# Performance work log

Hardware: AMD Instinct MI355X
Metric: run time of the kernel (lower is better)

Reference implementation:

```python
import jax, jax.numpy as jnp
import numpy as np

N = 1_000_000
C = 128
B = 16  # number of instances (batch segments)
EPS = 1e-5


def setup_inputs() -> dict:
    key = jax.random.key(0)
    k1, k2 = jax.random.split(key)
    x = jax.random.normal(k1, (N, C), dtype=jnp.float32)
    batch_idx = jnp.sort(jax.random.randint(k2, (N,), 0, B, dtype=jnp.int32))
    weight = jnp.ones((1, C), dtype=jnp.float32)
    bias = jnp.zeros((1, C), dtype=jnp.float32)
    return {"x": x, "batch_idx": batch_idx, "weight": weight, "bias": bias}


def reference(x, batch_idx, weight, bias):
    # per-instance counts [B, 1]
    cnt = jax.ops.segment_sum(jnp.ones((x.shape[0], 1), x.dtype), batch_idx,
                              num_segments=B)
    cnt = jnp.maximum(cnt, 1.0)
    # segment mean [B, C]
    mean = jax.ops.segment_sum(x, batch_idx, num_segments=B) / cnt
    centered = x - mean[batch_idx]               # broadcast-add of -mean
    # segment mean of squared centered features -> per-instance variance [B, C]
    var = jax.ops.segment_sum(centered * centered, batch_idx, num_segments=B) / cnt
    instd = 1.0 / jnp.sqrt(var + EPS)            # [B, C]
    # broadcast-multiply, then affine
    return centered * instd[batch_idx] * weight + bias
```

## Files before the change

kernel.cpp:

```cpp
#include <hip/hip_runtime.h>

#define CC 128
#define BSEG 16
#define EPSV 1e-5f
#define ROWS_PER_BLOCK 512
#define NORM_GRID 2048

typedef float v4f __attribute__((ext_vector_type(4)));

__device__ __forceinline__ v4f vmax0(v4f a)
{
    v4f r; r.x = fmaxf(a.x, 0.f); r.y = fmaxf(a.y, 0.f);
    r.z = fmaxf(a.z, 0.f); r.w = fmaxf(a.w, 0.f); return r;
}
__device__ __forceinline__ v4f vrsqrt_eps(v4f a)
{
    v4f r; r.x = rsqrtf(a.x + EPSV); r.y = rsqrtf(a.y + EPSV);
    r.z = rsqrtf(a.z + EPSV); r.w = rsqrtf(a.w + EPSV); return r;
}

__global__ __launch_bounds__(256) void ms_stats(const float* __restrict__ x,
                                                const int* __restrict__ bidx,
                                                int n,
                                                float* __restrict__ sum,
                                                float* __restrict__ sumsq,
                                                float* __restrict__ cnt)
{
    const int r0 = blockIdx.x * ROWS_PER_BLOCK;
    if (r0 >= n) return;
    const int rend = min(r0 + ROWS_PER_BLOCK, n);
    const int tq = threadIdx.x & 31;
    const int tr = threadIdx.x >> 5;

    const int seg_first = bidx[r0];
    const int seg_last  = bidx[rend - 1];

    v4f s = {0.f, 0.f, 0.f, 0.f};
    v4f q = {0.f, 0.f, 0.f, 0.f};

    if (seg_first == seg_last) {
        int r = r0 + tr;
        for (; r + 8 < rend; r += 16) {
            const v4f a = *reinterpret_cast<const v4f*>(x + (size_t)r * CC + tq * 4);
            const v4f b = *reinterpret_cast<const v4f*>(x + (size_t)(r + 8) * CC + tq * 4);
            s += a; q += a * a;
            s += b; q += b * b;
        }
        if (r < rend) {
            const v4f a = *reinterpret_cast<const v4f*>(x + (size_t)r * CC + tq * 4);
            s += a; q += a * a;
        }
        __shared__ float red[8][8][32];
        red[tr][0][tq] = s.x; red[tr][1][tq] = s.y; red[tr][2][tq] = s.z; red[tr][3][tq] = s.w;
        red[tr][4][tq] = q.x; red[tr][5][tq] = q.y; red[tr][6][tq] = q.z; red[tr][7][tq] = q.w;
        __syncthreads();
        const int j = threadIdx.x >> 5;
        float acc = 0.f;
        #pragma unroll
        for (int k = 0; k < 8; ++k) acc += red[k][j][tq];
        const int ch = tq * 4 + (j & 3);
        atomicAdd(((j < 4) ? sum : sumsq) + seg_first * CC + ch, acc);
        if (threadIdx.x == 0)
            atomicAdd(cnt + seg_first, (float)(rend - r0));
    } else {
        int cur = -1;
        float rows = 0.f;
        for (int r = r0 + tr; r < rend; r += 8) {
            const int seg = bidx[r];
            if (seg != cur) {
                if (cur >= 0) {
                    float* sd = sum   + cur * CC + tq * 4;
                    float* qd = sumsq + cur * CC + tq * 4;
                    atomicAdd(sd + 0, s.x); atomicAdd(sd + 1, s.y);
                    atomicAdd(sd + 2, s.z); atomicAdd(sd + 3, s.w);
                    atomicAdd(qd + 0, q.x); atomicAdd(qd + 1, q.y);
                    atomicAdd(qd + 2, q.z); atomicAdd(qd + 3, q.w);
                    if (tq == 0) atomicAdd(cnt + cur, rows);
                    s = (v4f){0.f, 0.f, 0.f, 0.f};
                    q = (v4f){0.f, 0.f, 0.f, 0.f};
                    rows = 0.f;
                }
                cur = seg;
            }
            const v4f a = *reinterpret_cast<const v4f*>(x + (size_t)r * CC + tq * 4);
            s += a; q += a * a;
            rows += 1.f;
        }
        if (cur >= 0) {
            float* sd = sum   + cur * CC + tq * 4;
            float* qd = sumsq + cur * CC + tq * 4;
            atomicAdd(sd + 0, s.x); atomicAdd(sd + 1, s.y);
            atomicAdd(sd + 2, s.z); atomicAdd(sd + 3, s.w);
            atomicAdd(qd + 0, q.x); atomicAdd(qd + 1, q.y);
            atomicAdd(qd + 2, q.z); atomicAdd(qd + 3, q.w);
            if (tq == 0) atomicAdd(cnt + cur, rows);
        }
    }
}

__global__ __launch_bounds__(256) void ms_norm(const float* __restrict__ x,
                                               const int* __restrict__ bidx,
                                               const float* __restrict__ sum,
                                               const float* __restrict__ sumsq,
                                               const float* __restrict__ cnt,
                                               const float* __restrict__ w,
                                               const float* __restrict__ bias,
                                               float* __restrict__ out,
                                               int n)
{
    const int npairs = n * 16;
    const int chunk  = (npairs + (int)gridDim.x - 1) / (int)gridDim.x;
    const int hi     = npairs - (int)blockIdx.x * chunk;
    if (hi <= 0) return;
    const int lo     = max(hi - chunk, 0);
    const int tid    = (int)threadIdx.x;

    const int c0 = ((hi + tid) & 15) * 8;
    const v4f w0 = *reinterpret_cast<const v4f*>(w + c0);
    const v4f w1 = *reinterpret_cast<const v4f*>(w + c0 + 4);
    const v4f b0 = *reinterpret_cast<const v4f*>(bias + c0);
    const v4f b1 = *reinterpret_cast<const v4f*>(bias + c0 + 4);

    int cur = -1;
    v4f sc0, sc1, sh0, sh1;

    for (int p = hi - 256 + tid; p >= lo; p -= 256) {
        const int r   = p >> 4;
        const int seg = bidx[r];
        if (seg != cur) {
            cur = seg;
            const int gi  = seg * CC + c0;
            const v4f su0 = *reinterpret_cast<const v4f*>(sum + gi);
            const v4f su1 = *reinterpret_cast<const v4f*>(sum + gi + 4);
            const v4f sq0 = *reinterpret_cast<const v4f*>(sumsq + gi);
            const v4f sq1 = *reinterpret_cast<const v4f*>(sumsq + gi + 4);
            const float rn = 1.0f / fmaxf(cnt[seg], 1.0f);
            const v4f m0 = su0 * rn;
            const v4f m1 = su1 * rn;
            const v4f is0 = vrsqrt_eps(vmax0(sq0 * rn - m0 * m0));
            const v4f is1 = vrsqrt_eps(vmax0(sq1 * rn - m1 * m1));
            sc0 = is0 * w0; sc1 = is1 * w1;
            sh0 = b0 - m0 * sc0; sh1 = b1 - m1 * sc1;
        }
        const float* px = x + (size_t)p * 8;
        const v4f a = *reinterpret_cast<const v4f*>(px);
        const v4f b = *reinterpret_cast<const v4f*>(px + 4);
        v4f o0, o1;
        o0.x = fmaf(a.x, sc0.x, sh0.x); o0.y = fmaf(a.y, sc0.y, sh0.y);
        o0.z = fmaf(a.z, sc0.z, sh0.z); o0.w = fmaf(a.w, sc0.w, sh0.w);
        o1.x = fmaf(b.x, sc1.x, sh1.x); o1.y = fmaf(b.y, sc1.y, sh1.y);
        o1.z = fmaf(b.z, sc1.z, sh1.z); o1.w = fmaf(b.w, sc1.w, sh1.w);
        float* po = out + (size_t)p * 8;
        __builtin_nontemporal_store(o0, reinterpret_cast<v4f*>(po));
        __builtin_nontemporal_store(o1, reinterpret_cast<v4f*>(po + 4));
    }
}

extern "C" void kernel_launch(void* const* d_in, const int* in_sizes, int n_in,
                              void* d_out, int out_size, void* d_ws, size_t ws_size,
                              hipStream_t stream)
{
    const float* x    = (const float*)d_in[0];
    const int*   bidx = (const int*)d_in[1];
    const float* w    = (const float*)d_in[2];
    const float* bias = (const float*)d_in[3];
    float* out = (float*)d_out;
    const int n = in_sizes[1];

    float* ws    = (float*)d_ws;
    float* sum   = ws;
    float* sumsq = ws + BSEG * CC;
    float* cnt   = ws + 2 * BSEG * CC;

    (void)hipMemsetAsync(d_ws, 0, (size_t)(2 * BSEG * CC + BSEG) * sizeof(float), stream);

    const int g1 = (n + ROWS_PER_BLOCK - 1) / ROWS_PER_BLOCK;
    ms_stats<<<g1, 256, 0, stream>>>(x, bidx, n, sum, sumsq, cnt);
    ms_norm<<<NORM_GRID, 256, 0, stream>>>(x, bidx, sum, sumsq, cnt, w, bias, out, n);
}
```

Before: 345.2 us.

## Precompute per-segment scale/shift in LDS and unroll grid-stride normalize loop

Each norm block first computes the scale and shift for all 16 segments and 128 channels into shared memory. It then processes the tensor with a grid-stride loop unrolled four times, walking backward, with loads hoisted ahead of the FMAs. This removes the per-thread branch that recomputed stats whenever a segment changed and exposes more memory-level parallelism. The cost is a 2048-element prologue per block and a less contiguous per-block access pattern than the old chunked layout.

```diff
diff --git a/kernel.cpp b/kernel.cpp
--- a/kernel.cpp
+++ b/kernel.cpp
@@ -7,17 +7,6 @@
 #define NORM_GRID 2048
 
 typedef float v4f __attribute__((ext_vector_type(4)));
-
-__device__ __forceinline__ v4f vmax0(v4f a)
-{
-    v4f r; r.x = fmaxf(a.x, 0.f); r.y = fmaxf(a.y, 0.f);
-    r.z = fmaxf(a.z, 0.f); r.w = fmaxf(a.w, 0.f); return r;
-}
-__device__ __forceinline__ v4f vrsqrt_eps(v4f a)
-{
-    v4f r; r.x = rsqrtf(a.x + EPSV); r.y = rsqrtf(a.y + EPSV);
-    r.z = rsqrtf(a.z + EPSV); r.w = rsqrtf(a.w + EPSV); return r;
-}
 
 __global__ __launch_bounds__(256) void ms_stats(const float* __restrict__ x,
                                                 const int* __restrict__ bidx,
@@ -108,51 +97,104 @@
                                                float* __restrict__ out,
                                                int n)
 {
-    const int npairs = n * 16;
-    const int chunk  = (npairs + (int)gridDim.x - 1) / (int)gridDim.x;
-    const int hi     = npairs - (int)blockIdx.x * chunk;
-    if (hi <= 0) return;
-    const int lo     = max(hi - chunk, 0);
-    const int tid    = (int)threadIdx.x;
-
-    const int c0 = ((hi + tid) & 15) * 8;
-    const v4f w0 = *reinterpret_cast<const v4f*>(w + c0);
-    const v4f w1 = *reinterpret_cast<const v4f*>(w + c0 + 4);
-    const v4f b0 = *reinterpret_cast<const v4f*>(bias + c0);
-    const v4f b1 = *reinterpret_cast<const v4f*>(bias + c0 + 4);
-
-    int cur = -1;
-    v4f sc0, sc1, sh0, sh1;
-
-    for (int p = hi - 256 + tid; p >= lo; p -= 256) {
-        const int r   = p >> 4;
-        const int seg = bidx[r];
-        if (seg != cur) {
-            cur = seg;
-            const int gi  = seg * CC + c0;
-            const v4f su0 = *reinterpret_cast<const v4f*>(sum + gi);
-            const v4f su1 = *reinterpret_cast<const v4f*>(sum + gi + 4);
-            const v4f sq0 = *reinterpret_cast<const v4f*>(sumsq + gi);
-            const v4f sq1 = *reinterpret_cast<const v4f*>(sumsq + gi + 4);
-            const float rn = 1.0f / fmaxf(cnt[seg], 1.0f);
-            const v4f m0 = su0 * rn;
-            const v4f m1 = su1 * rn;
-            const v4f is0 = vrsqrt_eps(vmax0(sq0 * rn - m0 * m0));
-            const v4f is1 = vrsqrt_eps(vmax0(sq1 * rn - m1 * m1));
-            sc0 = is0 * w0; sc1 = is1 * w1;
-            sh0 = b0 - m0 * sc0; sh1 = b1 - m1 * sc1;
-        }
-        const float* px = x + (size_t)p * 8;
-        const v4f a = *reinterpret_cast<const v4f*>(px);
-        const v4f b = *reinterpret_cast<const v4f*>(px + 4);
-        v4f o0, o1;
-        o0.x = fmaf(a.x, sc0.x, sh0.x); o0.y = fmaf(a.y, sc0.y, sh0.y);
-        o0.z = fmaf(a.z, sc0.z, sh0.z); o0.w = fmaf(a.w, sc0.w, sh0.w);
-        o1.x = fmaf(b.x, sc1.x, sh1.x); o1.y = fmaf(b.y, sc1.y, sh1.y);
-        o1.z = fmaf(b.z, sc1.z, sh1.z); o1.w = fmaf(b.w, sc1.w, sh1.w);
-        float* po = out + (size_t)p * 8;
-        __builtin_nontemporal_store(o0, reinterpret_cast<v4f*>(po));
-        __builtin_nontemporal_store(o1, reinterpret_cast<v4f*>(po + 4));
+    __shared__ v4f s_scale[BSEG * 32];
+    __shared__ v4f s_shift[BSEG * 32];
+    for (int i = threadIdx.x; i < BSEG * CC; i += 256) {
+        const int b = i >> 7;
+        const int c = i & (CC - 1);
+        const float nn   = fmaxf(cnt[b], 1.0f);
+        const float mean = sum[i] / nn;
+        const float var  = fmaxf(sumsq[i] / nn - mean * mean, 0.0f);
+        const float sc   = rsqrtf(var + EPSV) * w[c];
+        reinterpret_cast<float*>(s_scale)[i] = sc;
+        reinterpret_cast<float*>(s_shift)[i] = fmaf(-mean, sc, bias[c]);
+    }
+    __syncthreads();
+
+    const int total = n * 16;
+    const int T     = (int)(gridDim.x * blockDim.x);
+
+    int p = total - 1 - (int)(blockIdx.x * blockDim.x + threadIdx.x);
+
+    for (; p >= 3 * T; p -= 4 * T) {
+        const int p0 = p, p1 = p - T, p2 = p - 2 * T, p3 = p - 3 * T;
+        const int g0 = bidx[p0 >> 4];
+        const int g1 = bidx[p1 >> 4];
+        const int g2 = bidx[p2 >> 4];
+        const int g3 = bidx[p3 >> 4];
+        const v4f a0 = reinterpret_cast<const v4f*>(x)[2 * (size_t)p0];
+        const v4f b0 = reinterpret_cast<const v4f*>(x)[2 * (size_t)p0 + 1];
+        const v4f a1 = reinterpret_cast<const v4f*>(x)[2 * (size_t)p1];
+        const v4f b1 = reinterpret_cast<const v4f*>(x)[2 * (size_t)p1 + 1];
+        const v4f a2 = reinterpret_cast<const v4f*>(x)[2 * (size_t)p2];
+        const v4f b2 = reinterpret_cast<const v4f*>(x)[2 * (size_t)p2 + 1];
+        const v4f a3 = reinterpret_cast<const v4f*>(x)[2 * (size_t)p3];
+        const v4f b3 = reinterpret_cast<const v4f*>(x)[2 * (size_t)p3 + 1];
+
+        {
+            const int q2i = (p0 & 15) * 2;
+            const v4f sca = s_scale[g0 * 32 + q2i], scb = s_scale[g0 * 32 + q2i + 1];
+            const v4f sha = s_shift[g0 * 32 + q2i], shb = s_shift[g0 * 32 + q2i + 1];
+            v4f oa, ob;
+            oa.x = fmaf(a0.x, sca.x, sha.x); oa.y = fmaf(a0.y, sca.y, sha.y);
+            oa.z = fmaf(a0.z, sca.z, sha.z); oa.w = fmaf(a0.w, sca.w, sha.w);
+            ob.x = fmaf(b0.x, scb.x, shb.x); ob.y = fmaf(b0.y, scb.y, shb.y);
+            ob.z = fmaf(b0.z, scb.z, shb.z); ob.w = fmaf(b0.w, scb.w, shb.w);
+            __builtin_nontemporal_store(oa, reinterpret_cast<v4f*>(out) + 2 * (size_t)p0);
+            __builtin_nontemporal_store(ob, reinterpret_cast<v4f*>(out) + 2 * (size_t)p0 + 1);
+        }
+        {
+            const int q2i = (p1 & 15) * 2;
+            const v4f sca = s_scale[g1 * 32 + q2i], scb = s_scale[g1 * 32 + q2i + 1];
+            const v4f sha = s_shift[g1 * 32 + q2i], shb = s_shift[g1 * 32 + q2i + 1];
+            v4f oa, ob;
+            oa.x = fmaf(a1.x, sca.x, sha.x); oa.y = fmaf(a1.y, sca.y, sha.y);
+            oa.z = fmaf(a1.z, sca.z, sha.z); oa.w = fmaf(a1.w, sca.w, sha.w);
+            ob.x = fmaf(b1.x, scb.x, shb.x); ob.y = fmaf(b1.y, scb.y, shb.y);
+            ob.z = fmaf(b1.z, scb.z, shb.z); ob.w = fmaf(b1.w, scb.w, shb.w);
+            __builtin_nontemporal_store(oa, reinterpret_cast<v4f*>(out) + 2 * (size_t)p1);
+            __builtin_nontemporal_store(ob, reinterpret_cast<v4f*>(out) + 2 * (size_t)p1 + 1);
+        }
+        {
+            const int q2i = (p2 & 15) * 2;
+            const v4f sca = s_scale[g2 * 32 + q2i], scb = s_scale[g2 * 32 + q2i + 1];
+            const v4f sha = s_shift[g2 * 32 + q2i], shb = s_shift[g2 * 32 + q2i + 1];
+            v4f oa, ob;
+            oa.x = fmaf(a2.x, sca.x, sha.x); oa.y = fmaf(a2.y, sca.y, sha.y);
+            oa.z = fmaf(a2.z, sca.z, sha.z); oa.w = fmaf(a2.w, sca.w, sha.w);
+            ob.x = fmaf(b2.x, scb.x, shb.x); ob.y = fmaf(b2.y, scb.y, shb.y);
+            ob.z = fmaf(b2.z, scb.z, shb.z); ob.w = fmaf(b2.w, scb.w, shb.w);
+            __builtin_nontemporal_store(oa, reinterpret_cast<v4f*>(out) + 2 * (size_t)p2);
+            __builtin_nontemporal_store(ob, reinterpret_cast<v4f*>(out) + 2 * (size_t)p2 + 1);
+        }
+        {
+            const int q2i = (p3 & 15) * 2;
+            const v4f sca = s_scale[g3 * 32 + q2i], scb = s_scale[g3 * 32 + q2i + 1];
+            const v4f sha = s_shift[g3 * 32 + q2i], shb = s_shift[g3 * 32 + q2i + 1];
+            v4f oa, ob;
+            oa.x = fmaf(a3.x, sca.x, sha.x); oa.y = fmaf(a3.y, sca.y, sha.y);
+            oa.z = fmaf(a3.z, sca.z, sha.z); oa.w = fmaf(a3.w, sca.w, sha.w);
+            ob.x = fmaf(b3.x, scb.x, shb.x); ob.y = fmaf(b3.y, scb.y, shb.y);
+            ob.z = fmaf(b3.z, scb.z, shb.z); ob.w = fmaf(b3.w, scb.w, shb.w);
+            __builtin_nontemporal_store(oa, reinterpret_cast<v4f*>(out) + 2 * (size_t)p3);
+            __builtin_nontemporal_store(ob, reinterpret_cast<v4f*>(out) + 2 * (size_t)p3 + 1);
+        }
+    }
+
+    for (; p >= 0; p -= T) {
+        const int g = bidx[p >> 4];
+        const v4f a = reinterpret_cast<const v4f*>(x)[2 * (size_t)p];
+        const v4f b = reinterpret_cast<const v4f*>(x)[2 * (size_t)p + 1];
+        const int q2i = (p & 15) * 2;
+        const v4f sca = s_scale[g * 32 + q2i], scb = s_scale[g * 32 + q2i + 1];
+        const v4f sha = s_shift[g * 32 + q2i], shb = s_shift[g * 32 + q2i + 1];
+        v4f oa, ob;
+        oa.x = fmaf(a.x, sca.x, sha.x); oa.y = fmaf(a.y, sca.y, sha.y);
+        oa.z = fmaf(a.z, sca.z, sha.z); oa.w = fmaf(a.w, sca.w, sha.w);
+        ob.x = fmaf(b.x, scb.x, shb.x); ob.y = fmaf(b.y, scb.y, shb.y);
+        ob.z = fmaf(b.z, scb.z, shb.z); ob.w = fmaf(b.w, scb.w, shb.w);
+        __builtin_nontemporal_store(oa, reinterpret_cast<v4f*>(out) + 2 * (size_t)p);
+        __builtin_nontemporal_store(ob, reinterpret_cast<v4f*>(out) + 2 * (size_t)p + 1);
     }
 }
 
```

After: 354.0 us. +2.6%, slower.
